# Optimization experiments

Hardware: AMD Instinct MI355X
Metric: run time of the kernel (lower is better)

## Reference

```python
import jax, jax.numpy as jnp
import numpy as np

N_NODES = 50000
N_EDGES = 800000
IN_FEATS = 128
OUT_FEATS = 128


def mean_agg(feat, src, dst, num_nodes):
    # DGL copy_u + mean reduce: mean of in-neighbor (src) features per dst node;
    # nodes with zero in-degree get 0.
    msg = feat[src]                                        # [E, D] gather
    summed = jax.ops.segment_sum(msg, dst, num_segments=num_nodes)  # [N, D]
    deg = jax.ops.segment_sum(jnp.ones((src.shape[0],), feat.dtype), dst,
                              num_segments=num_nodes)      # [N]
    return summed / jnp.maximum(deg, 1.0)[:, None]


def setup_inputs() -> dict:
    key = jax.random.key(0)
    ks = jax.random.split(key, 16)
    sx = 1.0 / np.sqrt(IN_FEATS)
    sh = 1.0 / np.sqrt(OUT_FEATS)
    inp = {
        "x": jax.random.normal(ks[0], (N_NODES, IN_FEATS), jnp.float32),
        "h": jax.random.normal(ks[1], (N_NODES, OUT_FEATS), jnp.float32),
        "c": jax.random.normal(ks[2], (N_NODES, OUT_FEATS), jnp.float32),
        # stacked weights for the 4 gates (order: i, f, c, o)
        "Wx_self": jax.random.normal(ks[3], (4, IN_FEATS, OUT_FEATS), jnp.float32) * sx,
        "Wx_neigh": jax.random.normal(ks[4], (4, IN_FEATS, OUT_FEATS), jnp.float32) * sx,
        "Wh_self": jax.random.normal(ks[5], (4, OUT_FEATS, OUT_FEATS), jnp.float32) * sh,
        "Wh_neigh": jax.random.normal(ks[6], (4, OUT_FEATS, OUT_FEATS), jnp.float32) * sh,
        "w_ci": jax.random.uniform(ks[7], (OUT_FEATS,), jnp.float32),
        "w_cf": jax.random.uniform(ks[8], (OUT_FEATS,), jnp.float32),
        "w_co": jax.random.uniform(ks[9], (OUT_FEATS,), jnp.float32),
        "b_i": jax.random.uniform(ks[10], (OUT_FEATS,), jnp.float32),
        "b_f": jax.random.uniform(ks[11], (OUT_FEATS,), jnp.float32),
        "b_c": jax.random.uniform(ks[12], (OUT_FEATS,), jnp.float32),
        "b_o": jax.random.uniform(ks[13], (OUT_FEATS,), jnp.float32),
        "src": jax.random.randint(ks[14], (N_EDGES,), 0, N_NODES, jnp.int32),
        "dst": jax.random.randint(ks[15], (N_EDGES,), 0, N_NODES, jnp.int32),
    }
    return inp


def reference(x, h, c, Wx_self, Wx_neigh, Wh_self, Wh_neigh,
              w_ci, w_cf, w_co, b_i, b_f, b_c, b_o, src, dst):
    n = x.shape[0]
    # reuse_gate_rz=True: compute the two mean-aggregations once, shared by all nets
    h_N = mean_agg(x, src, dst, n)      # neighbor mean of x  [N, in]
    h_agg = mean_agg(h, src, dst, n)    # neighbor mean of h  [N, out]

    # each sub-net: net(g, feat, h_N=agg) = feat @ W_self + agg @ W_neigh
    # batched over the 4 gates (i, f, c, o)
    gx = jnp.einsum('ni,gio->gno', x, Wx_self) + jnp.einsum('ni,gio->gno', h_N, Wx_neigh)
    gh = jnp.einsum('no,goe->gne', h, Wh_self) + jnp.einsum('no,goe->gne', h_agg, Wh_neigh)
    s = gx + gh                          # [4, N, out]

    i = jax.nn.sigmoid(s[0] + w_ci * c + b_i)
    f = jax.nn.sigmoid(s[1] + w_cf * c + b_f)
    c_tilde = jnp.tanh(s[2] + b_c)
    new_c = f * c + i * c_tilde
    o = jax.nn.sigmoid(s[3] + w_co * new_c + b_o)
    new_h = o * jnp.tanh(new_c)
    return new_h, new_c
```

## Files before the change

### kernel.cpp

```cpp
#include <hip/hip_runtime.h>
#include <hip/hip_bf16.h>
#include <stdint.h>

#define N_NODES 50000
#define N_EDGES 800000
#define D 128
#define NPAD 50048
#define HKD 256
#define KDIM 512

typedef __attribute__((ext_vector_type(8))) __bf16 bf16x8;
typedef __attribute__((ext_vector_type(4))) __bf16 bf16x4;
typedef __attribute__((ext_vector_type(4))) float f32x4;
typedef __attribute__((ext_vector_type(2))) float f32x2;

__device__ __forceinline__ void gload_lds16(const void* g, void* l) {
  __builtin_amdgcn_global_load_lds(
      (const __attribute__((address_space(1))) unsigned int*)(uintptr_t)g,
      (__attribute__((address_space(3))) unsigned int*)(uint32_t)(uintptr_t)l,
      16, 0, 0);
}

__device__ __forceinline__ float sigm(float v) { return 1.0f / (1.0f + __expf(-v)); }
__device__ __forceinline__ float tanh_fast(float v) { return 1.0f - 2.0f / (1.0f + __expf(2.0f * v)); }

#if defined(__has_builtin) && __has_builtin(__builtin_amdgcn_cvt_pk_fp8_f32) && __has_builtin(__builtin_amdgcn_cvt_pk_f32_fp8)
__device__ __forceinline__ unsigned pack_fp8x4(float a, float b, float c, float d) {
  int p = __builtin_amdgcn_cvt_pk_fp8_f32(a, b, 0, false);
  p = __builtin_amdgcn_cvt_pk_fp8_f32(c, d, p, true);
  return (unsigned)p;
}
__device__ __forceinline__ f32x2 unpk_fp8_lo(unsigned u) { return __builtin_amdgcn_cvt_pk_f32_fp8(u, false); }
__device__ __forceinline__ f32x2 unpk_fp8_hi(unsigned u) { return __builtin_amdgcn_cvt_pk_f32_fp8(u, true); }
#else
#include <hip/hip_fp8.h>
__device__ __forceinline__ unsigned pack_fp8x4(float a, float b, float c, float d) {
  __hip_fp8_e4m3 qa(a), qb(b), qc(c), qd(d);
  return (unsigned)qa.__x | ((unsigned)qb.__x << 8) | ((unsigned)qc.__x << 16) | ((unsigned)qd.__x << 24);
}
__device__ __forceinline__ float unpk1(unsigned byte) {
  __hip_fp8_e4m3 t; t.__x = (__hip_fp8_storage_t)byte; return (float)t;
}
__device__ __forceinline__ f32x2 unpk_fp8_lo(unsigned u) { f32x2 r; r.x = unpk1(u & 0xff); r.y = unpk1((u >> 8) & 0xff); return r; }
__device__ __forceinline__ f32x2 unpk_fp8_hi(unsigned u) { f32x2 r; r.x = unpk1((u >> 16) & 0xff); r.y = unpk1(u >> 24); return r; }
#endif

#define NB_DEG 3125
#define NB_TOB 6250
#define NB_PKW 1024
__global__ void k_pre(const int* __restrict__ dst, int* __restrict__ deg,
                      const float* __restrict__ x, const float* __restrict__ h,
                      uint8_t* __restrict__ XH8,
                      const float* __restrict__ Wx_self, const float* __restrict__ Wx_neigh,
                      const float* __restrict__ Wh_self, const float* __restrict__ Wh_neigh,
                      __bf16* __restrict__ Wp) {
  int b = blockIdx.x;
  if (b < NB_DEG) {
    int e = b * 256 + threadIdx.x;
    atomicAdd(&deg[dst[e]], 1);
  } else if (b < NB_DEG + NB_TOB) {
    int idx = (b - NB_DEG) * 256 + threadIdx.x;
    int node = idx >> 5;
    int f4 = (idx & 31) << 2;
    float4 xv = *(const float4*)(x + (size_t)node * D + f4);
    float4 hv = *(const float4*)(h + (size_t)node * D + f4);
    uint8_t* r = XH8 + (size_t)node * HKD;
    *(unsigned*)(r + f4) = pack_fp8x4(xv.x, xv.y, xv.z, xv.w);
    *(unsigned*)(r + 128 + f4) = pack_fp8x4(hv.x, hv.y, hv.z, hv.w);
  } else {
    int idx = (b - NB_DEG - NB_TOB) * 256 + threadIdx.x;
    int e = idx & 7;
    int r16 = (idx >> 3) & 15;
    int q = (idx >> 7) & 3;
    int s = (idx >> 9) & 15;
    int G = idx >> 13;
    int wrow = G * 16 + r16;
    int g = wrow >> 7, o = wrow & 127;
    int k = s * 32 + q * 8 + e;
    const float* src; int i;
    if (k < 128)      { src = Wx_self;  i = k; }
    else if (k < 256) { src = Wh_self;  i = k - 128; }
    else if (k < 384) { src = Wx_neigh; i = k - 256; }
    else              { src = Wh_neigh; i = k - 384; }
    Wp[idx] = (__bf16)src[(g << 14) + (i << 7) + o];
  }
}

__global__ __launch_bounds__(1024) void k_scan(const int* __restrict__ deg, int* __restrict__ offs,
                                               int* __restrict__ cursor, int n) {
  const int t = threadIdx.x;
  const int lane = t & 63;
  const int w = t >> 6;
  __shared__ int wsum[16];
  __shared__ int carry_s;
  int carry = 0;
  for (int base = 0; base < n; base += 4096) {
    int idx = base + t * 4;
    int4 v = make_int4(0, 0, 0, 0);
    if (idx < n) v = *(const int4*)(deg + idx);
    int tsum = v.x + v.y + v.z + v.w;
    int s = tsum;
#pragma unroll
    for (int d = 1; d < 64; d <<= 1) {
      int u = __shfl_up(s, d, 64);
      if (lane >= d) s += u;
    }
    if (lane == 63) wsum[w] = s;
    __syncthreads();
    int woff = 0;
    for (int i = 0; i < w; i++) woff += wsum[i];
    int excl = carry + woff + (s - tsum);
    if (idx < n) {
      int4 o;
      o.x = excl; o.y = excl + v.x; o.z = o.y + v.y; o.w = o.z + v.z;
      *(int4*)(offs + idx) = o;
      *(int4*)(cursor + idx) = o;
    }
    __syncthreads();
    if (t == 0) {
      int tot = carry;
#pragma unroll
      for (int i = 0; i < 16; i++) tot += wsum[i];
      carry_s = tot;
    }
    __syncthreads();
    carry = carry_s;
  }
  if (t == 0) offs[n] = carry;
}

__global__ void k_fill(const int* __restrict__ src, const int* __restrict__ dst,
                       int* __restrict__ cursor, int* __restrict__ bins) {
  int e = blockIdx.x * 256 + threadIdx.x;
  if (e < N_EDGES) {
    int d = dst[e];
    int p = atomicAdd(&cursor[d], 1);
    bins[p] = src[e];
  }
}

__global__ void k_gather(const int* __restrict__ offs, const int* __restrict__ bins,
                         const uint8_t* __restrict__ XH8, __bf16* __restrict__ ZM) {
  int wid = (blockIdx.x * 256 + threadIdx.x) >> 6;
  int lane = threadIdx.x & 63;
  if (wid >= NPAD) return;
  if (wid >= N_NODES) {
    ((uint2*)(ZM + (size_t)wid * HKD))[lane] = make_uint2(0, 0);
    return;
  }
  const int half = lane >> 5;
  const int li = lane & 31;
  const int boff = li * 8;
  int beg = offs[wid], end = offs[wid + 1];
  float a[8] = {0.f, 0.f, 0.f, 0.f, 0.f, 0.f, 0.f, 0.f};
  auto acc = [&](uint2 v) {
    f32x2 p;
    p = unpk_fp8_lo(v.x); a[0] += p.x; a[1] += p.y;
    p = unpk_fp8_hi(v.x); a[2] += p.x; a[3] += p.y;
    p = unpk_fp8_lo(v.y); a[4] += p.x; a[5] += p.y;
    p = unpk_fp8_hi(v.y); a[6] += p.x; a[7] += p.y;
  };
  int j = beg + half;
  for (; j + 6 < end; j += 8) {
    int s0 = bins[j], s1 = bins[j + 2], s2 = bins[j + 4], s3 = bins[j + 6];
    uint2 v0 = *(const uint2*)(XH8 + (size_t)s0 * HKD + boff);
    uint2 v1 = *(const uint2*)(XH8 + (size_t)s1 * HKD + boff);
    uint2 v2 = *(const uint2*)(XH8 + (size_t)s2 * HKD + boff);
    uint2 v3 = *(const uint2*)(XH8 + (size_t)s3 * HKD + boff);
    acc(v0); acc(v1); acc(v2); acc(v3);
  }
  for (; j < end; j += 2) {
    uint2 v = *(const uint2*)(XH8 + (size_t)bins[j] * HKD + boff);
    acc(v);
  }
#pragma unroll
  for (int e = 0; e < 8; ++e) a[e] += __shfl_xor(a[e], 32, 64);
  int degn = end - beg;
  float inv = 1.0f / (float)(degn > 0 ? degn : 1);
  if (lane < 32) {
    bf16x8 bb;
#pragma unroll
    for (int e = 0; e < 8; ++e) bb[e] = (__bf16)(a[e] * inv);
    *(bf16x8*)(ZM + (size_t)wid * HKD + boff) = bb;
  }
}

__global__ __launch_bounds__(512, 4) void k_gemm(
    const float* __restrict__ xg, const float* __restrict__ hg,
    const __bf16* __restrict__ ZM, const __bf16* __restrict__ Wp,
    const float* __restrict__ c,
    const float* __restrict__ w_ci, const float* __restrict__ w_cf, const float* __restrict__ w_co,
    const float* __restrict__ b_i, const float* __restrict__ b_f, const float* __restrict__ b_c,
    const float* __restrict__ b_o,
    float* __restrict__ out_h, float* __restrict__ out_c) {
  __shared__ __align__(16) __bf16 As[4096 * 8];
  const int t = threadIdx.x;
  const int lane = t & 63;
  const int w = t >> 6;
  const int m0 = blockIdx.x * 64;
  const int l15 = lane & 15;
  const int q = lane >> 4;

#pragma unroll
  for (int i = 0; i < 4; ++i) {
    int u = i * 512 + t;
    int row = u >> 5, cz = u & 31;
    int cg = cz ^ (row & 7);
    gload_lds16(ZM + (size_t)(m0 + row) * HKD + cg * 8, (__bf16*)As + (2048 + u) * 8);
  }
#pragma unroll
  for (int i = 0; i < 4; ++i) {
    int u = i * 512 + t;
    int row = u >> 5, cs = u & 31;
    int slot = row * 32 + (cs ^ (row & 7));
    int grow = m0 + row;
    bf16x8 val;
#pragma unroll
    for (int e = 0; e < 8; ++e) val[e] = (__bf16)0.f;
    if (grow < N_NODES) {
      const float* sp = (cs < 16) ? (xg + (size_t)grow * D + cs * 8)
                                  : (hg + (size_t)grow * D + (cs - 16) * 8);
      float4 u0 = *(const float4*)sp;
      float4 u1 = *(const float4*)(sp + 4);
      val[0] = (__bf16)u0.x; val[1] = (__bf16)u0.y; val[2] = (__bf16)u0.z; val[3] = (__bf16)u0.w;
      val[4] = (__bf16)u1.x; val[5] = (__bf16)u1.y; val[6] = (__bf16)u1.z; val[7] = (__bf16)u1.w;
    }
    *(bf16x8*)((__bf16*)As + slot * 8) = val;
  }
  __syncthreads();

  f32x4 acc[4][4];
#pragma unroll
  for (int m = 0; m < 4; ++m)
#pragma unroll
    for (int g = 0; g < 4; ++g) acc[m][g] = (f32x4){0.f, 0.f, 0.f, 0.f};

  const __bf16* wp = Wp + (size_t)(w * 16) * 512 + lane * 8;

  auto LOADA = [&](int step, bf16x8* af) {
    const int base = (step < 8) ? 0 : 2048;
    const int cq = ((step < 8) ? step * 4 : (step - 8) * 4) + q;
#pragma unroll
    for (int m = 0; m < 4; ++m) {
      int row = m * 16 + l15;
      af[m] = *(const bf16x8*)((__bf16*)As + (base + row * 32 + (cq ^ (row & 7))) * 8);
    }
  };

  bf16x8 bA[4], bB[4];
#pragma unroll
  for (int g = 0; g < 4; ++g) bA[g] = *(const bf16x8*)(wp + g * 65536);

#pragma unroll
  for (int s2 = 0; s2 < 8; ++s2) {
    {
      const int step = 2 * s2;
#pragma unroll
      for (int g = 0; g < 4; ++g)
        bB[g] = *(const bf16x8*)(wp + g * 65536 + (step + 1) * 512);
      bf16x8 af[4];
      LOADA(step, af);
      __builtin_amdgcn_s_setprio(1);
#pragma unroll
      for (int m = 0; m < 4; ++m)
#pragma unroll
        for (int g = 0; g < 4; ++g)
          acc[m][g] = __builtin_amdgcn_mfma_f32_16x16x32_bf16(af[m], bA[g], acc[m][g], 0, 0, 0);
      __builtin_amdgcn_s_setprio(0);
    }
    {
      const int step = 2 * s2 + 1;
      if (step < 15) {
#pragma unroll
        for (int g = 0; g < 4; ++g)
          bA[g] = *(const bf16x8*)(wp + g * 65536 + (step + 1) * 512);
      }
      bf16x8 af[4];
      LOADA(step, af);
      __builtin_amdgcn_s_setprio(1);
#pragma unroll
      for (int m = 0; m < 4; ++m)
#pragma unroll
        for (int g = 0; g < 4; ++g)
          acc[m][g] = __builtin_amdgcn_mfma_f32_16x16x32_bf16(af[m], bB[g], acc[m][g], 0, 0, 0);
      __builtin_amdgcn_s_setprio(0);
    }
  }

  const int o = w * 16 + l15;
  const float wci = w_ci[o], wcf = w_cf[o], wco = w_co[o];
  const float bi = b_i[o], bfv = b_f[o], bc = b_c[o], bo = b_o[o];
#pragma unroll
  for (int m = 0; m < 4; ++m) {
#pragma unroll
    for (int r = 0; r < 4; ++r) {
      int row = m0 + m * 16 + q * 4 + r;
      if (row < N_NODES) {
        float cv = c[(size_t)row * D + o];
        float ig = sigm(acc[m][0][r] + wci * cv + bi);
        float fg = sigm(acc[m][1][r] + wcf * cv + bfv);
        float ct = tanh_fast(acc[m][2][r] + bc);
        float nc = fg * cv + ig * ct;
        float og = sigm(acc[m][3][r] + wco * nc + bo);
        out_h[(size_t)row * D + o] = og * tanh_fast(nc);
        out_c[(size_t)row * D + o] = nc;
      }
    }
  }
}

extern "C" void kernel_launch(void* const* d_in, const int* in_sizes, int n_in,
                              void* d_out, int out_size, void* d_ws, size_t ws_size,
                              hipStream_t stream) {
  const float* x = (const float*)d_in[0];
  const float* h = (const float*)d_in[1];
  const float* c = (const float*)d_in[2];
  const float* Wx_self = (const float*)d_in[3];
  const float* Wx_neigh = (const float*)d_in[4];
  const float* Wh_self = (const float*)d_in[5];
  const float* Wh_neigh = (const float*)d_in[6];
  const float* w_ci = (const float*)d_in[7];
  const float* w_cf = (const float*)d_in[8];
  const float* w_co = (const float*)d_in[9];
  const float* b_i = (const float*)d_in[10];
  const float* b_f = (const float*)d_in[11];
  const float* b_c = (const float*)d_in[12];
  const float* b_o = (const float*)d_in[13];
  const int* src = (const int*)d_in[14];
  const int* dst = (const int*)d_in[15];

  char* ws = (char*)d_ws;
  int* deg = (int*)(ws);
  int* offs = (int*)(ws + 200704);
  int* cursor = (int*)(ws + 400896);
  int* bins = (int*)(ws + 601088);
  uint8_t* XH8 = (uint8_t*)(ws + 4194304);
  __bf16* ZM = (__bf16*)(ws + 17039360);
  __bf16* Wp = (__bf16*)(ws + 42729472);

  float* out_h = (float*)d_out;
  float* out_c = out_h + (size_t)N_NODES * D;

  hipMemsetAsync(deg, 0, N_NODES * sizeof(int), stream);
  k_pre<<<NB_DEG + NB_TOB + NB_PKW, 256, 0, stream>>>(dst, deg, x, h, XH8,
                                                      Wx_self, Wx_neigh, Wh_self, Wh_neigh, Wp);
  k_scan<<<1, 1024, 0, stream>>>(deg, offs, cursor, N_NODES);
  k_fill<<<(N_EDGES + 255) / 256, 256, 0, stream>>>(src, dst, cursor, bins);
  k_gather<<<NPAD / 4, 256, 0, stream>>>(offs, bins, XH8, ZM);
  k_gemm<<<NPAD / 64, 512, 0, stream>>>(x, h, ZM, Wp, c, w_ci, w_cf, w_co,
                                        b_i, b_f, b_c, b_o, out_h, out_c);
}
```

Baseline: 219.1 us.

## Fuse neighbor-mean gather into GEMM kernel and precompute bf16 self features

Removes the separate gather kernel and its ZM intermediate. Each GEMM block now computes the fp8 neighbor means for its 64 rows directly into shared memory before running the MFMA loop. The pre-pass also writes a bf16 copy of x and h, padded to NPAD rows, so the GEMM can stream its self-feature operand into LDS asynchronously instead of converting fp32 in registers. This saves a kernel launch and the global round trip of the aggregated features. In exchange, the irregular gather latency now sits inside the GEMM block with less parallelism per node, which may reduce latency hiding.

```diff
diff --git a/kernel.cpp b/kernel.cpp
--- a/kernel.cpp
+++ b/kernel.cpp
@@ -46,11 +46,11 @@
 #endif
 
 #define NB_DEG 3125
-#define NB_TOB 6250
+#define NB_TOB 6256
 #define NB_PKW 1024
 __global__ void k_pre(const int* __restrict__ dst, int* __restrict__ deg,
                       const float* __restrict__ x, const float* __restrict__ h,
-                      uint8_t* __restrict__ XH8,
+                      __bf16* __restrict__ XHb, uint8_t* __restrict__ XH8,
                       const float* __restrict__ Wx_self, const float* __restrict__ Wx_neigh,
                       const float* __restrict__ Wh_self, const float* __restrict__ Wh_neigh,
                       __bf16* __restrict__ Wp) {
@@ -62,11 +62,20 @@
     int idx = (b - NB_DEG) * 256 + threadIdx.x;
     int node = idx >> 5;
     int f4 = (idx & 31) << 2;
-    float4 xv = *(const float4*)(x + (size_t)node * D + f4);
-    float4 hv = *(const float4*)(h + (size_t)node * D + f4);
-    uint8_t* r = XH8 + (size_t)node * HKD;
-    *(unsigned*)(r + f4) = pack_fp8x4(xv.x, xv.y, xv.z, xv.w);
-    *(unsigned*)(r + 128 + f4) = pack_fp8x4(hv.x, hv.y, hv.z, hv.w);
+    float4 xv = make_float4(0.f, 0.f, 0.f, 0.f), hv = make_float4(0.f, 0.f, 0.f, 0.f);
+    if (node < N_NODES) {
+      xv = *(const float4*)(x + (size_t)node * D + f4);
+      hv = *(const float4*)(h + (size_t)node * D + f4);
+    }
+    bf16x4 a, bb;
+    a[0] = (__bf16)xv.x; a[1] = (__bf16)xv.y; a[2] = (__bf16)xv.z; a[3] = (__bf16)xv.w;
+    bb[0] = (__bf16)hv.x; bb[1] = (__bf16)hv.y; bb[2] = (__bf16)hv.z; bb[3] = (__bf16)hv.w;
+    __bf16* br = XHb + (size_t)node * HKD;
+    *(bf16x4*)(br + f4) = a;
+    *(bf16x4*)(br + 128 + f4) = bb;
+    uint8_t* r8 = XH8 + (size_t)node * HKD;
+    *(unsigned*)(r8 + f4) = pack_fp8x4(xv.x, xv.y, xv.z, xv.w);
+    *(unsigned*)(r8 + 128 + f4) = pack_fp8x4(hv.x, hv.y, hv.z, hv.w);
   } else {
     int idx = (b - NB_DEG - NB_TOB) * 256 + threadIdx.x;
     int e = idx & 7;
@@ -139,55 +148,10 @@
   }
 }
 
-__global__ void k_gather(const int* __restrict__ offs, const int* __restrict__ bins,
-                         const uint8_t* __restrict__ XH8, __bf16* __restrict__ ZM) {
-  int wid = (blockIdx.x * 256 + threadIdx.x) >> 6;
-  int lane = threadIdx.x & 63;
-  if (wid >= NPAD) return;
-  if (wid >= N_NODES) {
-    ((uint2*)(ZM + (size_t)wid * HKD))[lane] = make_uint2(0, 0);
-    return;
-  }
-  const int half = lane >> 5;
-  const int li = lane & 31;
-  const int boff = li * 8;
-  int beg = offs[wid], end = offs[wid + 1];
-  float a[8] = {0.f, 0.f, 0.f, 0.f, 0.f, 0.f, 0.f, 0.f};
-  auto acc = [&](uint2 v) {
-    f32x2 p;
-    p = unpk_fp8_lo(v.x); a[0] += p.x; a[1] += p.y;
-    p = unpk_fp8_hi(v.x); a[2] += p.x; a[3] += p.y;
-    p = unpk_fp8_lo(v.y); a[4] += p.x; a[5] += p.y;
-    p = unpk_fp8_hi(v.y); a[6] += p.x; a[7] += p.y;
-  };
-  int j = beg + half;
-  for (; j + 6 < end; j += 8) {
-    int s0 = bins[j], s1 = bins[j + 2], s2 = bins[j + 4], s3 = bins[j + 6];
-    uint2 v0 = *(const uint2*)(XH8 + (size_t)s0 * HKD + boff);
-    uint2 v1 = *(const uint2*)(XH8 + (size_t)s1 * HKD + boff);
-    uint2 v2 = *(const uint2*)(XH8 + (size_t)s2 * HKD + boff);
-    uint2 v3 = *(const uint2*)(XH8 + (size_t)s3 * HKD + boff);
-    acc(v0); acc(v1); acc(v2); acc(v3);
-  }
-  for (; j < end; j += 2) {
-    uint2 v = *(const uint2*)(XH8 + (size_t)bins[j] * HKD + boff);
-    acc(v);
-  }
-#pragma unroll
-  for (int e = 0; e < 8; ++e) a[e] += __shfl_xor(a[e], 32, 64);
-  int degn = end - beg;
-  float inv = 1.0f / (float)(degn > 0 ? degn : 1);
-  if (lane < 32) {
-    bf16x8 bb;
-#pragma unroll
-    for (int e = 0; e < 8; ++e) bb[e] = (__bf16)(a[e] * inv);
-    *(bf16x8*)(ZM + (size_t)wid * HKD + boff) = bb;
-  }
-}
-
 __global__ __launch_bounds__(512, 4) void k_gemm(
-    const float* __restrict__ xg, const float* __restrict__ hg,
-    const __bf16* __restrict__ ZM, const __bf16* __restrict__ Wp,
+    const __bf16* __restrict__ XHb, const uint8_t* __restrict__ XH8,
+    const int* __restrict__ offs, const int* __restrict__ bins,
+    const __bf16* __restrict__ Wp,
     const float* __restrict__ c,
     const float* __restrict__ w_ci, const float* __restrict__ w_cf, const float* __restrict__ w_co,
     const float* __restrict__ b_i, const float* __restrict__ b_f, const float* __restrict__ b_c,
@@ -206,26 +170,47 @@
     int u = i * 512 + t;
     int row = u >> 5, cz = u & 31;
     int cg = cz ^ (row & 7);
-    gload_lds16(ZM + (size_t)(m0 + row) * HKD + cg * 8, (__bf16*)As + (2048 + u) * 8);
-  }
-#pragma unroll
-  for (int i = 0; i < 4; ++i) {
-    int u = i * 512 + t;
-    int row = u >> 5, cs = u & 31;
-    int slot = row * 32 + (cs ^ (row & 7));
-    int grow = m0 + row;
-    bf16x8 val;
-#pragma unroll
-    for (int e = 0; e < 8; ++e) val[e] = (__bf16)0.f;
-    if (grow < N_NODES) {
-      const float* sp = (cs < 16) ? (xg + (size_t)grow * D + cs * 8)
-                                  : (hg + (size_t)grow * D + (cs - 16) * 8);
-      float4 u0 = *(const float4*)sp;
-      float4 u1 = *(const float4*)(sp + 4);
-      val[0] = (__bf16)u0.x; val[1] = (__bf16)u0.y; val[2] = (__bf16)u0.z; val[3] = (__bf16)u0.w;
-      val[4] = (__bf16)u1.x; val[5] = (__bf16)u1.y; val[6] = (__bf16)u1.z; val[7] = (__bf16)u1.w;
-    }
-    *(bf16x8*)((__bf16*)As + slot * 8) = val;
+    gload_lds16(XHb + (size_t)(m0 + row) * HKD + cg * 8, (__bf16*)As + (size_t)u * 8);
+  }
+
+  const __bf16* wp = Wp + (size_t)(w * 16) * 512 + lane * 8;
+  bf16x8 bA[4], bB[4];
+#pragma unroll
+  for (int g = 0; g < 4; ++g) bA[g] = *(const bf16x8*)(wp + g * 65536);
+
+#pragma unroll
+  for (int rnd = 0; rnd < 4; ++rnd) {
+    int row = rnd * 16 + w * 2 + (lane >> 5);
+    int node = m0 + row;
+    int li = lane & 31;
+    float a[8] = {0.f, 0.f, 0.f, 0.f, 0.f, 0.f, 0.f, 0.f};
+    float a2[8] = {0.f, 0.f, 0.f, 0.f, 0.f, 0.f, 0.f, 0.f};
+    int beg = 0, end = 0;
+    if (node < N_NODES) { beg = offs[node]; end = offs[node + 1]; }
+    const uint8_t* xb = XH8 + li * 8;
+    auto acc8 = [&](uint2 v, float* aa) {
+      f32x2 p;
+      p = unpk_fp8_lo(v.x); aa[0] += p.x; aa[1] += p.y;
+      p = unpk_fp8_hi(v.x); aa[2] += p.x; aa[3] += p.y;
+      p = unpk_fp8_lo(v.y); aa[4] += p.x; aa[5] += p.y;
+      p = unpk_fp8_hi(v.y); aa[6] += p.x; aa[7] += p.y;
+    };
+    int j = beg;
+    for (; j + 1 < end; j += 2) {
+      uint2 v0 = *(const uint2*)(xb + (size_t)bins[j] * HKD);
+      uint2 v1 = *(const uint2*)(xb + (size_t)bins[j + 1] * HKD);
+      acc8(v0, a); acc8(v1, a2);
+    }
+    if (j < end) {
+      uint2 v0 = *(const uint2*)(xb + (size_t)bins[j] * HKD);
+      acc8(v0, a);
+    }
+    float inv = 1.0f / (float)((end - beg) > 0 ? (end - beg) : 1);
+    bf16x8 bb;
+#pragma unroll
+    for (int e = 0; e < 8; ++e) bb[e] = (__bf16)((a[e] + a2[e]) * inv);
+    int slot = 2048 + row * 32 + (li ^ (row & 7));
+    *(bf16x8*)((__bf16*)As + (size_t)slot * 8) = bb;
   }
   __syncthreads();
 
@@ -234,22 +219,16 @@
   for (int m = 0; m < 4; ++m)
 #pragma unroll
     for (int g = 0; g < 4; ++g) acc[m][g] = (f32x4){0.f, 0.f, 0.f, 0.f};
-
-  const __bf16* wp = Wp + (size_t)(w * 16) * 512 + lane * 8;
 
   auto LOADA = [&](int step, bf16x8* af) {
     const int base = (step < 8) ? 0 : 2048;
-    const int cq = ((step < 8) ? step * 4 : (step - 8) * 4) + q;
+    const int cq = ((step < 8) ? step : (step - 8)) * 4 + q;
 #pragma unroll
     for (int m = 0; m < 4; ++m) {
       int row = m * 16 + l15;
-      af[m] = *(const bf16x8*)((__bf16*)As + (base + row * 32 + (cq ^ (row & 7))) * 8);
+      af[m] = *(const bf16x8*)((__bf16*)As + (size_t)(base + row * 32 + (cq ^ (row & 7))) * 8);
     }
   };
-
-  bf16x8 bA[4], bB[4];
-#pragma unroll
-  for (int g = 0; g < 4; ++g) bA[g] = *(const bf16x8*)(wp + g * 65536);
 
 #pragma unroll
   for (int s2 = 0; s2 < 8; ++s2) {
@@ -335,18 +314,17 @@
   int* cursor = (int*)(ws + 400896);
   int* bins = (int*)(ws + 601088);
   uint8_t* XH8 = (uint8_t*)(ws + 4194304);
-  __bf16* ZM = (__bf16*)(ws + 17039360);
+  __bf16* XHb = (__bf16*)(ws + 17039360);
   __bf16* Wp = (__bf16*)(ws + 42729472);
 
   float* out_h = (float*)d_out;
   float* out_c = out_h + (size_t)N_NODES * D;
 
   hipMemsetAsync(deg, 0, N_NODES * sizeof(int), stream);
-  k_pre<<<NB_DEG + NB_TOB + NB_PKW, 256, 0, stream>>>(dst, deg, x, h, XH8,
+  k_pre<<<NB_DEG + NB_TOB + NB_PKW, 256, 0, stream>>>(dst, deg, x, h, XHb, XH8,
                                                       Wx_self, Wx_neigh, Wh_self, Wh_neigh, Wp);
   k_scan<<<1, 1024, 0, stream>>>(deg, offs, cursor, N_NODES);
   k_fill<<<(N_EDGES + 255) / 256, 256, 0, stream>>>(src, dst, cursor, bins);
-  k_gather<<<NPAD / 4, 256, 0, stream>>>(offs, bins, XH8, ZM);
-  k_gemm<<<NPAD / 64, 512, 0, stream>>>(x, h, ZM, Wp, c, w_ci, w_cf, w_co,
+  k_gemm<<<NPAD / 64, 512, 0, stream>>>(XHb, XH8, offs, bins, Wp, c, w_ci, w_cf, w_co,
                                         b_i, b_f, b_c, b_o, out_h, out_c);
 }
```

Measured after the change: 242.9 us. 10.9% more time.

## Pre-convert x/h to bf16 and stage all GEMM A-operands via async LDS loads

Applied to the files above, without the earlier changes.

k_pre now also writes a bf16 copy of x and h alongside the fp8 copy. k_gemm then fills its whole 64x512 A tile with global_load_lds, replacing the fp32 loads it converted in registers. The bf16 copies and the aggregated means are kept in the output buffers. Each GEMM block reads only its own rows before writing them, and the last block clamps its row index, so the zero-padding writes for the extra rows are dropped. This halves the GEMM's activation read traffic and frees its registers, at the cost of an extra bf16 write pass in k_pre and reliance on the in-place aliasing staying race-free.

```diff
diff --git a/kernel.cpp b/kernel.cpp
--- a/kernel.cpp
+++ b/kernel.cpp
@@ -50,7 +50,7 @@
 #define NB_PKW 1024
 __global__ void k_pre(const int* __restrict__ dst, int* __restrict__ deg,
                       const float* __restrict__ x, const float* __restrict__ h,
-                      uint8_t* __restrict__ XH8,
+                      __bf16* __restrict__ XHb, uint8_t* __restrict__ XH8,
                       const float* __restrict__ Wx_self, const float* __restrict__ Wx_neigh,
                       const float* __restrict__ Wh_self, const float* __restrict__ Wh_neigh,
                       __bf16* __restrict__ Wp) {
@@ -64,9 +64,15 @@
     int f4 = (idx & 31) << 2;
     float4 xv = *(const float4*)(x + (size_t)node * D + f4);
     float4 hv = *(const float4*)(h + (size_t)node * D + f4);
-    uint8_t* r = XH8 + (size_t)node * HKD;
-    *(unsigned*)(r + f4) = pack_fp8x4(xv.x, xv.y, xv.z, xv.w);
-    *(unsigned*)(r + 128 + f4) = pack_fp8x4(hv.x, hv.y, hv.z, hv.w);
+    bf16x4 a, bb;
+    a[0] = (__bf16)xv.x; a[1] = (__bf16)xv.y; a[2] = (__bf16)xv.z; a[3] = (__bf16)xv.w;
+    bb[0] = (__bf16)hv.x; bb[1] = (__bf16)hv.y; bb[2] = (__bf16)hv.z; bb[3] = (__bf16)hv.w;
+    __bf16* br = XHb + (size_t)node * HKD;
+    *(bf16x4*)(br + f4) = a;
+    *(bf16x4*)(br + 128 + f4) = bb;
+    uint8_t* r8 = XH8 + (size_t)node * HKD;
+    *(unsigned*)(r8 + f4) = pack_fp8x4(xv.x, xv.y, xv.z, xv.w);
+    *(unsigned*)(r8 + 128 + f4) = pack_fp8x4(hv.x, hv.y, hv.z, hv.w);
   } else {
     int idx = (b - NB_DEG - NB_TOB) * 256 + threadIdx.x;
     int e = idx & 7;
@@ -143,11 +149,7 @@
                          const uint8_t* __restrict__ XH8, __bf16* __restrict__ ZM) {
   int wid = (blockIdx.x * 256 + threadIdx.x) >> 6;
   int lane = threadIdx.x & 63;
-  if (wid >= NPAD) return;
-  if (wid >= N_NODES) {
-    ((uint2*)(ZM + (size_t)wid * HKD))[lane] = make_uint2(0, 0);
-    return;
-  }
+  if (wid >= N_NODES) return;
   const int half = lane >> 5;
   const int li = lane & 31;
   const int boff = li * 8;
@@ -186,14 +188,13 @@
 }
 
 __global__ __launch_bounds__(512, 4) void k_gemm(
-    const float* __restrict__ xg, const float* __restrict__ hg,
-    const __bf16* __restrict__ ZM, const __bf16* __restrict__ Wp,
+    const __bf16* __restrict__ XHb, const __bf16* __restrict__ ZM, const __bf16* __restrict__ Wp,
     const float* __restrict__ c,
     const float* __restrict__ w_ci, const float* __restrict__ w_cf, const float* __restrict__ w_co,
     const float* __restrict__ b_i, const float* __restrict__ b_f, const float* __restrict__ b_c,
     const float* __restrict__ b_o,
     float* __restrict__ out_h, float* __restrict__ out_c) {
-  __shared__ __align__(16) __bf16 As[4096 * 8];
+  __shared__ __align__(16) __bf16 As[64 * KDIM];
   const int t = threadIdx.x;
   const int lane = t & 63;
   const int w = t >> 6;
@@ -202,30 +203,15 @@
   const int q = lane >> 4;
 
 #pragma unroll
-  for (int i = 0; i < 4; ++i) {
-    int u = i * 512 + t;
-    int row = u >> 5, cz = u & 31;
-    int cg = cz ^ (row & 7);
-    gload_lds16(ZM + (size_t)(m0 + row) * HKD + cg * 8, (__bf16*)As + (2048 + u) * 8);
-  }
-#pragma unroll
-  for (int i = 0; i < 4; ++i) {
-    int u = i * 512 + t;
-    int row = u >> 5, cs = u & 31;
-    int slot = row * 32 + (cs ^ (row & 7));
+  for (int i = 0; i < 8; ++i) {
+    int s = i * 512 + t;
+    int row = s >> 6;
+    int cg = (s & 63) ^ (row & 7);
     int grow = m0 + row;
-    bf16x8 val;
-#pragma unroll
-    for (int e = 0; e < 8; ++e) val[e] = (__bf16)0.f;
-    if (grow < N_NODES) {
-      const float* sp = (cs < 16) ? (xg + (size_t)grow * D + cs * 8)
-                                  : (hg + (size_t)grow * D + (cs - 16) * 8);
-      float4 u0 = *(const float4*)sp;
-      float4 u1 = *(const float4*)(sp + 4);
-      val[0] = (__bf16)u0.x; val[1] = (__bf16)u0.y; val[2] = (__bf16)u0.z; val[3] = (__bf16)u0.w;
-      val[4] = (__bf16)u1.x; val[5] = (__bf16)u1.y; val[6] = (__bf16)u1.z; val[7] = (__bf16)u1.w;
-    }
-    *(bf16x8*)((__bf16*)As + slot * 8) = val;
+    if (grow >= N_NODES) grow = N_NODES - 1;
+    const __bf16* src = (cg < 32) ? (XHb + (size_t)grow * HKD + cg * 8)
+                                  : (ZM + (size_t)grow * HKD + (cg - 32) * 8);
+    gload_lds16(src, (__bf16*)As + (size_t)s * 8);
   }
   __syncthreads();
 
@@ -236,16 +222,6 @@
     for (int g = 0; g < 4; ++g) acc[m][g] = (f32x4){0.f, 0.f, 0.f, 0.f};
 
   const __bf16* wp = Wp + (size_t)(w * 16) * 512 + lane * 8;
-
-  auto LOADA = [&](int step, bf16x8* af) {
-    const int base = (step < 8) ? 0 : 2048;
-    const int cq = ((step < 8) ? step * 4 : (step - 8) * 4) + q;
-#pragma unroll
-    for (int m = 0; m < 4; ++m) {
-      int row = m * 16 + l15;
-      af[m] = *(const bf16x8*)((__bf16*)As + (base + row * 32 + (cq ^ (row & 7))) * 8);
-    }
-  };
 
   bf16x8 bA[4], bB[4];
 #pragma unroll
@@ -259,7 +235,12 @@
       for (int g = 0; g < 4; ++g)
         bB[g] = *(const bf16x8*)(wp + g * 65536 + (step + 1) * 512);
       bf16x8 af[4];
-      LOADA(step, af);
+#pragma unroll
+      for (int m = 0; m < 4; ++m) {
+        int row = m * 16 + l15;
+        int cl = (step * 4 + q) ^ (row & 7);
+        af[m] = *(const bf16x8*)(As + ((size_t)row * 64 + cl) * 8);
+      }
       __builtin_amdgcn_s_setprio(1);
 #pragma unroll
       for (int m = 0; m < 4; ++m)
@@ -276,7 +257,12 @@
           bA[g] = *(const bf16x8*)(wp + g * 65536 + (step + 1) * 512);
       }
       bf16x8 af[4];
-      LOADA(step, af);
+#pragma unroll
+      for (int m = 0; m < 4; ++m) {
+        int row = m * 16 + l15;
+        int cl = (step * 4 + q) ^ (row & 7);
+        af[m] = *(const bf16x8*)(As + ((size_t)row * 64 + cl) * 8);
+      }
       __builtin_amdgcn_s_setprio(1);
 #pragma unroll
       for (int m = 0; m < 4; ++m)
@@ -335,18 +321,19 @@
   int* cursor = (int*)(ws + 400896);
   int* bins = (int*)(ws + 601088);
   uint8_t* XH8 = (uint8_t*)(ws + 4194304);
-  __bf16* ZM = (__bf16*)(ws + 17039360);
-  __bf16* Wp = (__bf16*)(ws + 42729472);
+  __bf16* Wp = (__bf16*)(ws + 17039360);
 
   float* out_h = (float*)d_out;
   float* out_c = out_h + (size_t)N_NODES * D;
+  __bf16* XHb = (__bf16*)out_h;
+  __bf16* ZM = (__bf16*)out_c;
 
   hipMemsetAsync(deg, 0, N_NODES * sizeof(int), stream);
-  k_pre<<<NB_DEG + NB_TOB + NB_PKW, 256, 0, stream>>>(dst, deg, x, h, XH8,
+  k_pre<<<NB_DEG + NB_TOB + NB_PKW, 256, 0, stream>>>(dst, deg, x, h, XHb, XH8,
                                                       Wx_self, Wx_neigh, Wh_self, Wh_neigh, Wp);
   k_scan<<<1, 1024, 0, stream>>>(deg, offs, cursor, N_NODES);
   k_fill<<<(N_EDGES + 255) / 256, 256, 0, stream>>>(src, dst, cursor, bins);
-  k_gather<<<NPAD / 4, 256, 0, stream>>>(offs, bins, XH8, ZM);
-  k_gemm<<<NPAD / 64, 512, 0, stream>>>(x, h, ZM, Wp, c, w_ci, w_cf, w_co,
+  k_gather<<<(N_NODES + 3) / 4, 256, 0, stream>>>(offs, bins, XH8, ZM);
+  k_gemm<<<NPAD / 64, 512, 0, stream>>>(XHb, ZM, Wp, c, w_ci, w_cf, w_co,
                                         b_i, b_f, b_c, b_o, out_h, out_c);
 }
```

After: 208.7 us. 4.7% less time.
